# Optimization experiments

Measured on AMD Instinct MI355X. Metric: run time of the kernel, lower is better.

The kernel has to match this reference:

```python
import jax, jax.numpy as jnp
import numpy as np

N_HEADS = 16

def rotate_half(x):
    x1, x2 = jnp.split(x, 2, axis=-1)
    return jnp.concatenate([-x2, x1], axis=-1)

def setup_inputs() -> dict:
    key = jax.random.key(0)
    ks = jax.random.split(key, 6)
    dim = 2048
    B, T = 4, 2048
    x = jax.random.normal(ks[0], (B, T, dim), dtype=jnp.float32)
    pos = jnp.arange(T, dtype=jnp.float32).reshape(T, 1, 1)
    def w(k):
        return jax.random.normal(k, (dim, dim), dtype=jnp.float32) * 0.02
    return {
        "x": x, "pos": pos,
        "wq_w": w(ks[1]), "wq_b": jnp.zeros((dim,), jnp.float32),
        "wk_w": w(ks[2]), "wk_b": jnp.zeros((dim,), jnp.float32),
        "wv_w": w(ks[3]), "wv_b": jnp.zeros((dim,), jnp.float32),
        "wo_w": w(ks[4]), "wo_b": jnp.zeros((dim,), jnp.float32),
    }

def reference(x, pos, wq_w, wq_b, wk_w, wk_b, wv_w, wv_b, wo_w, wo_b):
    B, T, dim = x.shape
    H = N_HEADS
    hd = dim // H
    q = (x @ wq_w.T + wq_b).reshape(B, T, H, hd)
    k = (x @ wk_w.T + wk_b).reshape(B, T, H, hd)
    v = (x @ wv_w.T + wv_b).reshape(B, T, H, hd)
    # RoPE: freq over half the head dim, sin/cos tiled to full head dim
    freq = 1.0 / (10000.0 ** (jnp.arange(0, hd, 2, dtype=jnp.float32) / hd))  # [hd/2]
    ang = pos * freq                      # [T,1,hd/2]
    sin = jnp.concatenate([jnp.sin(ang), jnp.sin(ang)], axis=-1)  # [T,1,hd]
    cos = jnp.concatenate([jnp.cos(ang), jnp.cos(ang)], axis=-1)  # [T,1,hd]
    q = q * cos + rotate_half(q) * sin
    k = k * cos + rotate_half(k) * sin
    # [B,H,T,hd]
    q = q.transpose(0, 2, 1, 3)
    k = k.transpose(0, 2, 1, 3)
    v = v.transpose(0, 2, 1, 3)
    scale = 1.0 / np.sqrt(hd).astype(np.float32)
    attn = jnp.einsum('bhqd,bhkd->bhqk', q, k) * scale  # [B,H,T,T]
    attn = jax.nn.softmax(attn, axis=-1)
    out = jnp.einsum('bhqk,bhkd->bhqd', attn, v)        # [B,H,T,hd]
    out = out.transpose(0, 2, 1, 3).reshape(B, T, dim)
    return out @ wo_w.T + wo_b
```

## Files before the change

### kernel.cpp

```cpp
#include <hip/hip_runtime.h>


using floatx4  = __attribute__((ext_vector_type(4))) float;
using short8   = __attribute__((ext_vector_type(8))) short;
using ushortx4 = __attribute__((ext_vector_type(4))) unsigned short;

#define DEVFN static __device__ __forceinline__

DEVFN unsigned short f2bf(float f) {
  unsigned u = __builtin_bit_cast(unsigned, f);
  u += 0x7fffu + ((u >> 16) & 1u);
  return (unsigned short)(u >> 16);
}
DEVFN float bf2f(unsigned short h) {
  return __builtin_bit_cast(float, ((unsigned)h) << 16);
}

DEVFN void async_cp16(const unsigned short* g, unsigned short* l) {
  __builtin_amdgcn_global_load_lds(
      (const __attribute__((address_space(1))) void*)g,
      (__attribute__((address_space(3))) void*)l,
      16, 0, 0);
}

__global__ __launch_bounds__(256) void cast_kernel(const float4* __restrict__ in,
                                                   ushortx4* __restrict__ out) {
  long u = (long)blockIdx.x * 256 + threadIdx.x;
  float4 v = in[u];
  out[u] = (ushortx4){f2bf(v.x), f2bf(v.y), f2bf(v.z), f2bf(v.w)};
}

__global__ __launch_bounds__(256) void cs_table_kernel(const float* __restrict__ pos,
                                                       float2* __restrict__ cst) {
  int idx = blockIdx.x * 256 + threadIdx.x;
  int t = idx >> 6, j = idx & 63;
  float ang = pos[t] * exp2f(-0.20762051f * (float)j);
  cst[idx] = make_float2(cosf(ang), sinf(ang));
}

__global__ __launch_bounds__(512, 2) void qkv_gemm(
    const unsigned short* __restrict__ A,
    const unsigned short* __restrict__ Wq, const unsigned short* __restrict__ Wk,
    const unsigned short* __restrict__ Wv,
    const float* __restrict__ bq, const float* __restrict__ bk,
    const float* __restrict__ bv,
    unsigned short* __restrict__ Oq, unsigned short* __restrict__ Ok,
    unsigned short* __restrict__ Ov,
    const float2* __restrict__ cst) {
  constexpr int K = 2048;
  constexpr int NT = 64;
  __shared__ __align__(16) unsigned short lds[49152];
  const int tid = threadIdx.x;
  const int wave = tid >> 6, lane = tid & 63;
  const int ln15 = lane & 15, quad = lane >> 4;
  const int wm = wave >> 2, wn = wave & 3;
  const int bid = blockIdx.x;
  const int g = bid >> 8;
  const int b2 = bid & 255;
  const unsigned short* Bw = (g == 0) ? Wq : (g == 1) ? Wk : Wv;
  const float* bias = (g == 0) ? bq : (g == 1) ? bk : bv;
  unsigned short* Cout = (g == 0) ? Oq : (g == 1) ? Ok : Ov;
  const int xcd = b2 & 7, sl = b2 >> 3;
  const int m0 = (xcd * 4 + (sl & 3)) * 256;
  const int n0 = (sl >> 2) * 256;

  const unsigned short *srcA0, *srcA1, *srcB0, *srcB1;
  {
    int u = tid;
    int L = u >> 3, cc = (u & 7) ^ (L & 7);
    int row = L * 2 + (cc >> 2), col = (cc & 3) * 8;
    srcA0 = A + (long)(m0 + row) * K + col;
    srcB0 = Bw + (long)(n0 + row) * K + col;
  }
  {
    int u = tid + 512;
    int L = u >> 3, cc = (u & 7) ^ (L & 7);
    int row = L * 2 + (cc >> 2), col = (cc & 3) * 8;
    srcA1 = A + (long)(m0 + row) * K + col;
    srcB1 = Bw + (long)(n0 + row) * K + col;
  }
  const int sdst = wave * 512;

#define STAGE_G(t, bufp)                                                \
  do {                                                                  \
    async_cp16(srcA0 + (long)(t) * 32, (bufp) + sdst);                  \
    async_cp16(srcA1 + (long)(t) * 32, (bufp) + 4096 + sdst);           \
    async_cp16(srcB0 + (long)(t) * 32, (bufp) + 8192 + sdst);           \
    async_cp16(srcB1 + (long)(t) * 32, (bufp) + 12288 + sdst);          \
  } while (0)

  int offA[8], offB[4];
#pragma unroll
  for (int mi = 0; mi < 8; ++mi) {
    int row = wm * 128 + mi * 16 + ln15;
    int line = row >> 1, cc = (row & 1) * 4 + quad;
    offA[mi] = line * 64 + (cc ^ (line & 7)) * 8;
  }
#pragma unroll
  for (int nj = 0; nj < 4; ++nj) {
    int row = wn * 64 + nj * 16 + ln15;
    int line = row >> 1, cc = (row & 1) * 4 + quad;
    offB[nj] = 8192 + line * 64 + (cc ^ (line & 7)) * 8;
  }

  floatx4 acc[8][4];
#pragma unroll
  for (int i = 0; i < 8; ++i)
#pragma unroll
    for (int j = 0; j < 4; ++j) acc[i][j] = (floatx4){0.f, 0.f, 0.f, 0.f};

  unsigned short* const bA0 = lds;
  unsigned short* const bA1 = lds + 16384;
  unsigned short* const bA2 = lds + 32768;

  STAGE_G(0, bA0);
  STAGE_G(1, bA1);
  asm volatile("s_waitcnt vmcnt(4)" ::: "memory");
  __builtin_amdgcn_s_barrier();

  int cb = 0;
  for (int t = 0; t < NT; ++t) {
    unsigned short* cur = (cb == 0) ? bA0 : ((cb == 1) ? bA1 : bA2);
    if (t < NT - 2) {
      int nb = cb ? cb - 1 : 2;
      unsigned short* nxt = (nb == 0) ? bA0 : ((nb == 1) ? bA1 : bA2);
      STAGE_G(t + 2, nxt);
    }
    short8 af[8], bf4[4];
#pragma unroll
    for (int mi = 0; mi < 8; ++mi) af[mi] = *(const short8*)(cur + offA[mi]);
#pragma unroll
    for (int nj = 0; nj < 4; ++nj) bf4[nj] = *(const short8*)(cur + offB[nj]);
    __builtin_amdgcn_s_setprio(1);
#pragma unroll
    for (int mi = 0; mi < 8; ++mi)
#pragma unroll
      for (int nj = 0; nj < 4; ++nj)
        acc[mi][nj] = __builtin_amdgcn_mfma_f32_16x16x32_bf16(af[mi], bf4[nj],
                                                              acc[mi][nj], 0, 0, 0);
    __builtin_amdgcn_s_setprio(0);
    if (t < NT - 2) {
      asm volatile("s_waitcnt vmcnt(4)" ::: "memory");
    } else if (t == NT - 2) {
      asm volatile("s_waitcnt vmcnt(0)" ::: "memory");
    }
    __builtin_amdgcn_s_barrier();
    cb = (cb == 2) ? 0 : cb + 1;
  }
#undef STAGE_G

  const int b_ = m0 >> 11;
  const int t0m = m0 & 2047;
  const int h0 = n0 >> 7;

  if (g == 2) {
#pragma unroll
    for (int rnd = 0; rnd < 2; ++rnd) {
      __syncthreads();
      if (wm == rnd) {
#pragma unroll
        for (int nj = 0; nj < 4; ++nj) {
          int nloc = wn * 64 + nj * 16 + ln15;
          float bv = bias[n0 + nloc];
#pragma unroll
          for (int mi = 0; mi < 8; ++mi)
#pragma unroll
            for (int r = 0; r < 4; ++r) {
              int tl = mi * 16 + quad * 4 + r;
              int phys = (tl >> 3) ^ (nloc & 15);
              lds[nloc * 128 + phys * 8 + (tl & 7)] = f2bf(acc[mi][nj][r] + bv);
            }
        }
      }
      __syncthreads();
#pragma unroll
      for (int j = 0; j < 8; ++j) {
        int u = j * 512 + tid;
        int nloc = u >> 4, c = u & 15;
        int phys = c ^ (nloc & 15);
        int h = h0 + (nloc >> 7), d = nloc & 127;
        *(short8*)(Cout +
                   ((((long)(b_ * 16 + h)) << 7) + d) * 2048 + t0m + rnd * 128 + c * 8) =
            *(const short8*)(lds + nloc * 128 + phys * 8);
      }
    }
  } else {
#pragma unroll
    for (int rnd = 0; rnd < 2; ++rnd) {
      __syncthreads();
      if (wm == rnd) {
#pragma unroll
        for (int nj = 0; nj < 4; ++nj) {
          int nloc = wn * 64 + nj * 16 + ln15;
          float bv = bias[n0 + nloc];
#pragma unroll
          for (int mi = 0; mi < 8; ++mi)
#pragma unroll
            for (int r = 0; r < 4; ++r) {
              int tl = mi * 16 + quad * 4 + r;
              int phys = (nloc >> 3) ^ (tl & 15);
              lds[tl * 256 + phys * 8 + (nloc & 7)] = f2bf(acc[mi][nj][r] + bv);
            }
        }
      }
      __syncthreads();
#pragma unroll
      for (int j = 0; j < 8; ++j) {
        int u = j * 512 + tid;
        int tl = u >> 5, c = u & 31;
        int phys = c ^ (tl & 15);
        int hh = h0 + (c >> 4);
        int tt = t0m + rnd * 128 + tl;
        int cl = c & 15;
        int cp = (cl < 8) ? c + 8 : c - 8;
        int physp = cp ^ (tl & 15);
        short8 s8 = *(const short8*)(lds + tl * 256 + phys * 8);
        short8 p8 = *(const short8*)(lds + tl * 256 + physp * 8);
        const float2* ct = cst + tt * 64 + (cl & 7) * 8;
        short8 o8;
#pragma unroll
        for (int e = 0; e < 8; ++e) {
          float2 cs = ct[e];
          float x = bf2f((unsigned short)s8[e]);
          float y = bf2f((unsigned short)p8[e]);
          float v = (cl < 8) ? (x * cs.x - y * cs.y) : (x * cs.x + y * cs.y);
          o8[e] = (short)f2bf(v);
        }
        *(short8*)(Cout + ((((long)(b_ * 16 + hh)) << 11) + tt) * 128 + cl * 8) = o8;
      }
    }
  }
}

__global__ __launch_bounds__(512, 2) void gemm_wo(const unsigned short* __restrict__ A,
                                                  const unsigned short* __restrict__ Bw,
                                                  const float* __restrict__ bias,
                                                  float* __restrict__ Cout) {
  constexpr int K = 2048;
  constexpr int NT = 64;
  __shared__ __align__(16) unsigned short lds[49152];
  const int tid = threadIdx.x;
  const int wave = tid >> 6, lane = tid & 63;
  const int ln15 = lane & 15, quad = lane >> 4;
  const int wm = wave >> 2, wn = wave & 3;
  const int bid = blockIdx.x;
  const int xcd = bid & 7, sl = bid >> 3;
  const int m0 = (xcd * 4 + (sl & 3)) * 256;
  const int n0 = (sl >> 2) * 256;

  const unsigned short *srcA0, *srcA1, *srcB0, *srcB1;
  {
    int u = tid;
    int L = u >> 3, cc = (u & 7) ^ (L & 7);
    int row = L * 2 + (cc >> 2), col = (cc & 3) * 8;
    srcA0 = A + (long)(m0 + row) * K + col;
    srcB0 = Bw + (long)(n0 + row) * K + col;
  }
  {
    int u = tid + 512;
    int L = u >> 3, cc = (u & 7) ^ (L & 7);
    int row = L * 2 + (cc >> 2), col = (cc & 3) * 8;
    srcA1 = A + (long)(m0 + row) * K + col;
    srcB1 = Bw + (long)(n0 + row) * K + col;
  }
  const int sdst = wave * 512;

#define STAGE_G(t, bufp)                                                \
  do {                                                                  \
    async_cp16(srcA0 + (long)(t) * 32, (bufp) + sdst);                  \
    async_cp16(srcA1 + (long)(t) * 32, (bufp) + 4096 + sdst);           \
    async_cp16(srcB0 + (long)(t) * 32, (bufp) + 8192 + sdst);           \
    async_cp16(srcB1 + (long)(t) * 32, (bufp) + 12288 + sdst);          \
  } while (0)

  int offA[8], offB[4];
#pragma unroll
  for (int mi = 0; mi < 8; ++mi) {
    int row = wm * 128 + mi * 16 + ln15;
    int line = row >> 1, cc = (row & 1) * 4 + quad;
    offA[mi] = line * 64 + (cc ^ (line & 7)) * 8;
  }
#pragma unroll
  for (int nj = 0; nj < 4; ++nj) {
    int row = wn * 64 + nj * 16 + ln15;
    int line = row >> 1, cc = (row & 1) * 4 + quad;
    offB[nj] = 8192 + line * 64 + (cc ^ (line & 7)) * 8;
  }

  floatx4 acc[8][4];
#pragma unroll
  for (int i = 0; i < 8; ++i)
#pragma unroll
    for (int j = 0; j < 4; ++j) acc[i][j] = (floatx4){0.f, 0.f, 0.f, 0.f};

  unsigned short* const bA0 = lds;
  unsigned short* const bA1 = lds + 16384;
  unsigned short* const bA2 = lds + 32768;

  STAGE_G(0, bA0);
  STAGE_G(1, bA1);
  asm volatile("s_waitcnt vmcnt(4)" ::: "memory");
  __builtin_amdgcn_s_barrier();

  int cb = 0;
  for (int t = 0; t < NT; ++t) {
    unsigned short* cur = (cb == 0) ? bA0 : ((cb == 1) ? bA1 : bA2);
    if (t < NT - 2) {
      int nb = cb ? cb - 1 : 2;
      unsigned short* nxt = (nb == 0) ? bA0 : ((nb == 1) ? bA1 : bA2);
      STAGE_G(t + 2, nxt);
    }
    short8 af[8], bf4[4];
#pragma unroll
    for (int mi = 0; mi < 8; ++mi) af[mi] = *(const short8*)(cur + offA[mi]);
#pragma unroll
    for (int nj = 0; nj < 4; ++nj) bf4[nj] = *(const short8*)(cur + offB[nj]);
    __builtin_amdgcn_s_setprio(1);
#pragma unroll
    for (int mi = 0; mi < 8; ++mi)
#pragma unroll
      for (int nj = 0; nj < 4; ++nj)
        acc[mi][nj] = __builtin_amdgcn_mfma_f32_16x16x32_bf16(af[mi], bf4[nj],
                                                              acc[mi][nj], 0, 0, 0);
    __builtin_amdgcn_s_setprio(0);
    if (t < NT - 2) {
      asm volatile("s_waitcnt vmcnt(4)" ::: "memory");
    } else if (t == NT - 2) {
      asm volatile("s_waitcnt vmcnt(0)" ::: "memory");
    }
    __builtin_amdgcn_s_barrier();
    cb = (cb == 2) ? 0 : cb + 1;
  }
#undef STAGE_G

  float* lf = (float*)lds;
#pragma unroll
  for (int rnd = 0; rnd < 4; ++rnd) {
    __syncthreads();
    if (wm == (rnd >> 1)) {
#pragma unroll
      for (int nj = 0; nj < 4; ++nj) {
        int nloc = wn * 64 + nj * 16 + ln15;
        float bv = bias[n0 + nloc];
#pragma unroll
        for (int mh = 0; mh < 4; ++mh) {
          int mi = (rnd & 1) * 4 + mh;
#pragma unroll
          for (int r = 0; r < 4; ++r) {
            int tl = mh * 16 + quad * 4 + r;
            int phys = (nloc >> 2) ^ (tl & 15);
            lf[tl * 256 + phys * 4 + (nloc & 3)] = acc[mi][nj][r] + bv;
          }
        }
      }
    }
    __syncthreads();
#pragma unroll
    for (int j = 0; j < 8; ++j) {
      int u = j * 512 + tid;
      int tl = u >> 6, c = u & 63;
      int phys = c ^ (tl & 15);
      int m = m0 + rnd * 64 + tl;
      *(floatx4*)(Cout + (long)m * 2048 + n0 + c * 4) =
          *(const floatx4*)(lf + tl * 256 + phys * 4);
    }
  }
}

__global__ __launch_bounds__(512, 2) void flash_kernel(
    const unsigned short* __restrict__ Q,
    const unsigned short* __restrict__ Kmat,
    const unsigned short* __restrict__ Vt,
    unsigned short* __restrict__ Out) {
  constexpr int T = 2048;
  constexpr float SCALE = 0.08838834764831845f;
  __shared__ __align__(16) unsigned short lds[49152];

  const int tid = threadIdx.x;
  const int wave = tid >> 6, lane = tid & 63;
  const int ln15 = lane & 15, quad = lane >> 4;
  const int l7 = ln15 & 7;
  const int bid = blockIdx.x;
  const int xcd = bid & 7, sl = bid >> 3;
  const int bh = xcd * 8 + (sl >> 3);
  const int q0 = (sl & 7) * 256;

  const unsigned short* Qb = Q + (long)bh * T * 128;
  const unsigned short* Kb = Kmat + (long)bh * T * 128;
  const unsigned short* Vb = Vt + (long)bh * 128 * T;
  unsigned short* pw = lds + 32768 + wave * 2048;

  short8 qf[2][4];
#pragma unroll
  for (int mi = 0; mi < 2; ++mi)
#pragma unroll
    for (int ks = 0; ks < 4; ++ks)
      qf[mi][ks] = *(const short8*)(Qb + (long)(q0 + wave * 32 + mi * 16 + ln15) * 128 +
                                    ks * 32 + quad * 8);

#define STAGE_KV(t, kdst, vdst)                                                  \
  do {                                                                           \
    _Pragma("unroll") for (int j = 0; j < 2; ++j) {                              \
      int u = j * 512 + tid;                                                     \
      int row = u >> 4;                                                          \
      int c = (u & 15) ^ (row & 15);                                             \
      async_cp16(Kb + (long)((t) * 64 + row) * 128 + c * 8,                      \
                 (kdst) + (j * 512 + wave * 64) * 8);                            \
    }                                                                            \
    _Pragma("unroll") for (int j = 0; j < 2; ++j) {                              \
      int u = j * 512 + tid;                                                     \
      int row = u >> 3;                                                          \
      int c = (u & 7) ^ (row & 7);                                               \
      async_cp16(Vb + (long)row * T + (t) * 64 + c * 8,                          \
                 (vdst) + (j * 512 + wave * 64) * 8);                            \
    }                                                                            \
  } while (0)

  STAGE_KV(0, lds, lds + 16384);
  asm volatile("s_waitcnt vmcnt(0)" ::: "memory");
  __syncthreads();

  floatx4 oacc[2][8];
#pragma unroll
  for (int mi = 0; mi < 2; ++mi)
#pragma unroll
    for (int nj = 0; nj < 8; ++nj) oacc[mi][nj] = (floatx4){0.f, 0.f, 0.f, 0.f};
  float mst[2][4], lsp[2][4];
#pragma unroll
  for (int mi = 0; mi < 2; ++mi)
#pragma unroll
    for (int r = 0; r < 4; ++r) { mst[mi][r] = -1e30f; lsp[mi][r] = 0.f; }

  for (int t = 0; t < 32; ++t) {
    unsigned short* kc = lds + (t & 1) * 8192;
    unsigned short* vc = lds + 16384 + (t & 1) * 8192;
    if (t < 31) {
      unsigned short* kn = lds + ((t + 1) & 1) * 8192;
      unsigned short* vn = lds + 16384 + ((t + 1) & 1) * 8192;
      STAGE_KV(t + 1, kn, vn);
    }

    floatx4 sacc[2][4];
#pragma unroll
    for (int mi = 0; mi < 2; ++mi)
#pragma unroll
      for (int ni = 0; ni < 4; ++ni) sacc[mi][ni] = (floatx4){0.f, 0.f, 0.f, 0.f};
#pragma unroll
    for (int ks = 0; ks < 4; ++ks) {
      short8 bfr[4];
#pragma unroll
      for (int ni = 0; ni < 4; ++ni) {
        int row = ni * 16 + ln15;
        int phys = (ks * 4 + quad) ^ ln15;
        bfr[ni] = *(const short8*)(kc + row * 128 + phys * 8);
      }
      __builtin_amdgcn_s_setprio(1);
#pragma unroll
      for (int mi = 0; mi < 2; ++mi)
#pragma unroll
        for (int ni = 0; ni < 4; ++ni)
          sacc[mi][ni] = __builtin_amdgcn_mfma_f32_16x16x32_bf16(qf[mi][ks], bfr[ni],
                                                                 sacc[mi][ni], 0, 0, 0);
      __builtin_amdgcn_s_setprio(0);
    }

#pragma unroll
    for (int mi = 0; mi < 2; ++mi)
#pragma unroll
      for (int r = 0; r < 4; ++r) {
        float mx = fmaxf(fmaxf(sacc[mi][0][r], sacc[mi][1][r]),
                         fmaxf(sacc[mi][2][r], sacc[mi][3][r]));
#pragma unroll
        for (int off = 1; off < 16; off <<= 1) mx = fmaxf(mx, __shfl_xor(mx, off, 16));
        mx *= SCALE;
        float mold = mst[mi][r];
        float mnew = fmaxf(mold, mx);
        float alpha = __expf(mold - mnew);
        float rs = 0.f;
#pragma unroll
        for (int ni = 0; ni < 4; ++ni) {
          float p = __expf(sacc[mi][ni][r] * SCALE - mnew);
          sacc[mi][ni][r] = p;
          rs += p;
        }
        mst[mi][r] = mnew;
        lsp[mi][r] = lsp[mi][r] * alpha + rs;
#pragma unroll
        for (int nj = 0; nj < 8; ++nj) oacc[mi][nj][r] *= alpha;
      }

#pragma unroll
    for (int mi = 0; mi < 2; ++mi)
#pragma unroll
      for (int ni = 0; ni < 4; ++ni) {
        int cc = ni * 2 + (ln15 >> 3);
#pragma unroll
        for (int r = 0; r < 4; ++r) {
          int m = mi * 16 + quad * 4 + r;
          pw[m * 64 + (cc ^ (m & 7)) * 8 + l7] = f2bf(sacc[mi][ni][r]);
        }
      }

#pragma unroll
    for (int ks = 0; ks < 2; ++ks) {
      short8 af[2], bv[8];
#pragma unroll
      for (int mi = 0; mi < 2; ++mi) {
        int phys = (ks * 4 + quad) ^ l7;
        af[mi] = *(const short8*)(pw + (mi * 16 + ln15) * 64 + phys * 8);
      }
#pragma unroll
      for (int nj = 0; nj < 8; ++nj) {
        int row = nj * 16 + ln15;
        int phys = (ks * 4 + quad) ^ (row & 7);
        bv[nj] = *(const short8*)(vc + row * 64 + phys * 8);
      }
      __builtin_amdgcn_s_setprio(1);
#pragma unroll
      for (int mi = 0; mi < 2; ++mi)
#pragma unroll
        for (int nj = 0; nj < 8; ++nj)
          oacc[mi][nj] = __builtin_amdgcn_mfma_f32_16x16x32_bf16(af[mi], bv[nj],
                                                                 oacc[mi][nj], 0, 0, 0);
      __builtin_amdgcn_s_setprio(0);
    }

    asm volatile("s_waitcnt vmcnt(0)" ::: "memory");
    __syncthreads();
  }
#undef STAGE_KV

  float rinv[2][4];
#pragma unroll
  for (int mi = 0; mi < 2; ++mi)
#pragma unroll
    for (int r = 0; r < 4; ++r) {
      float l = lsp[mi][r];
#pragma unroll
      for (int off = 1; off < 16; off <<= 1) l += __shfl_xor(l, off, 16);
      rinv[mi][r] = 1.f / l;
    }
#pragma unroll
  for (int mi = 0; mi < 2; ++mi)
#pragma unroll
    for (int nj = 0; nj < 8; ++nj)
#pragma unroll
      for (int r = 0; r < 4; ++r)
        lds[(wave * 32 + mi * 16 + quad * 4 + r) * 128 + nj * 16 + ln15] =
            f2bf(oacc[mi][nj][r] * rinv[mi][r]);
  __syncthreads();
  const int b = bh >> 4, h = bh & 15;
  long obase = ((long)(b * T + q0) << 11) + h * 128;
#pragma unroll
  for (int j = 0; j < 8; ++j) {
    int u = j * 512 + tid;
    int r = u >> 4, c = u & 15;
    *(short8*)(Out + obase + ((long)r << 11) + c * 8) =
        *(const short8*)(lds + r * 128 + c * 8);
  }
}

extern "C" void kernel_launch(void* const* d_in, const int* in_sizes, int n_in,
                              void* d_out, int out_size, void* d_ws, size_t ws_size,
                              hipStream_t stream) {
  const float* x    = (const float*)d_in[0];
  const float* pos  = (const float*)d_in[1];
  const float* wq_w = (const float*)d_in[2];
  const float* wq_b = (const float*)d_in[3];
  const float* wk_w = (const float*)d_in[4];
  const float* wk_b = (const float*)d_in[5];
  const float* wv_w = (const float*)d_in[6];
  const float* wv_b = (const float*)d_in[7];
  const float* wo_w = (const float*)d_in[8];
  const float* wo_b = (const float*)d_in[9];

  unsigned short* xb  = (unsigned short*)d_ws;
  unsigned short* wqb = xb  + (1u << 24);
  unsigned short* wkb = wqb + (1u << 22);
  unsigned short* wvb = wkb + (1u << 22);
  unsigned short* wob = wvb + (1u << 22);
  unsigned short* qb  = wob + (1u << 22);
  unsigned short* kb  = qb  + (1u << 24);
  unsigned short* vtb = kb  + (1u << 24);
  unsigned short* ab  = vtb + (1u << 24);
  float2* cst = (float2*)ab;

  cast_kernel<<<16384, 256, 0, stream>>>((const float4*)x, (ushortx4*)xb);
  cast_kernel<<<4096, 256, 0, stream>>>((const float4*)wq_w, (ushortx4*)wqb);
  cast_kernel<<<4096, 256, 0, stream>>>((const float4*)wk_w, (ushortx4*)wkb);
  cast_kernel<<<4096, 256, 0, stream>>>((const float4*)wv_w, (ushortx4*)wvb);
  cast_kernel<<<4096, 256, 0, stream>>>((const float4*)wo_w, (ushortx4*)wob);
  cs_table_kernel<<<512, 256, 0, stream>>>(pos, cst);

  qkv_gemm<<<768, 512, 0, stream>>>(xb, wqb, wkb, wvb, wq_b, wk_b, wv_b,
                                    qb, kb, vtb, cst);
  flash_kernel<<<512, 512, 0, stream>>>(qb, kb, vtb, ab);
  gemm_wo<<<256, 512, 0, stream>>>(ab, wob, wo_b, (float*)d_out);
}
```

Before: 675.9 us.

## Fuse cast kernels, single-buffer K in flash attention, use exp2 softmax

Merges the five cast launches and the sin/cos table launch into one prep kernel to cut launch overhead. In flash attention, K is single-buffered, with the next tile's K load issued after the QK MMAs behind a barrier. This shrinks LDS from 96KB to 80KB, and launch bounds are raised to 4 blocks per CU to aim for higher occupancy. Softmax is switched to exp2 with the scale folded into log2e. The cost is less K prefetch overlap, an extra barrier per iteration, and tighter register limits that may cause spills.

```diff
diff --git a/kernel.cpp b/kernel.cpp
--- a/kernel.cpp
+++ b/kernel.cpp
@@ -23,19 +23,30 @@
       16, 0, 0);
 }
 
-__global__ __launch_bounds__(256) void cast_kernel(const float4* __restrict__ in,
-                                                   ushortx4* __restrict__ out) {
-  long u = (long)blockIdx.x * 256 + threadIdx.x;
-  float4 v = in[u];
-  out[u] = (ushortx4){f2bf(v.x), f2bf(v.y), f2bf(v.z), f2bf(v.w)};
-}
-
-__global__ __launch_bounds__(256) void cs_table_kernel(const float* __restrict__ pos,
-                                                       float2* __restrict__ cst) {
-  int idx = blockIdx.x * 256 + threadIdx.x;
-  int t = idx >> 6, j = idx & 63;
-  float ang = pos[t] * exp2f(-0.20762051f * (float)j);
-  cst[idx] = make_float2(cosf(ang), sinf(ang));
+__global__ __launch_bounds__(256) void prep_kernel(
+    const float4* __restrict__ x, const float4* __restrict__ wq,
+    const float4* __restrict__ wk, const float4* __restrict__ wv,
+    const float4* __restrict__ wo, const float* __restrict__ pos,
+    ushortx4* __restrict__ xb, ushortx4* __restrict__ wqb,
+    ushortx4* __restrict__ wkb, ushortx4* __restrict__ wvb,
+    ushortx4* __restrict__ wob, float2* __restrict__ cst) {
+  int bid = blockIdx.x;
+  if (bid < 32768) {
+    const float4* in; ushortx4* out; int base;
+    if (bid < 16384)      { in = x;  out = xb;  base = 0; }
+    else if (bid < 20480) { in = wq; out = wqb; base = 16384; }
+    else if (bid < 24576) { in = wk; out = wkb; base = 20480; }
+    else if (bid < 28672) { in = wv; out = wvb; base = 24576; }
+    else                  { in = wo; out = wob; base = 28672; }
+    long u = (long)(bid - base) * 256 + threadIdx.x;
+    float4 v = in[u];
+    out[u] = (ushortx4){f2bf(v.x), f2bf(v.y), f2bf(v.z), f2bf(v.w)};
+  } else {
+    int idx = (bid - 32768) * 256 + threadIdx.x;
+    int t = idx >> 6, j = idx & 63;
+    float ang = pos[t] * exp2f(-0.20762051f * (float)j);
+    cst[idx] = make_float2(cosf(ang), sinf(ang));
+  }
 }
 
 __global__ __launch_bounds__(512, 2) void qkv_gemm(
@@ -367,14 +378,14 @@
   }
 }
 
-__global__ __launch_bounds__(512, 2) void flash_kernel(
+__global__ __launch_bounds__(512, 4) void flash_kernel(
     const unsigned short* __restrict__ Q,
     const unsigned short* __restrict__ Kmat,
     const unsigned short* __restrict__ Vt,
     unsigned short* __restrict__ Out) {
   constexpr int T = 2048;
-  constexpr float SCALE = 0.08838834764831845f;
-  __shared__ __align__(16) unsigned short lds[49152];
+  constexpr float SL2E = 0.12754228f;
+  __shared__ __align__(16) unsigned short lds[40960];
 
   const int tid = threadIdx.x;
   const int wave = tid >> 6, lane = tid & 63;
@@ -388,7 +399,7 @@
   const unsigned short* Qb = Q + (long)bh * T * 128;
   const unsigned short* Kb = Kmat + (long)bh * T * 128;
   const unsigned short* Vb = Vt + (long)bh * 128 * T;
-  unsigned short* pw = lds + 32768 + wave * 2048;
+  unsigned short* pw = lds + 24576 + wave * 2048;
 
   short8 qf[2][4];
 #pragma unroll
@@ -398,15 +409,18 @@
       qf[mi][ks] = *(const short8*)(Qb + (long)(q0 + wave * 32 + mi * 16 + ln15) * 128 +
                                     ks * 32 + quad * 8);
 
-#define STAGE_KV(t, kdst, vdst)                                                  \
+#define STAGE_K(t)                                                               \
   do {                                                                           \
     _Pragma("unroll") for (int j = 0; j < 2; ++j) {                              \
       int u = j * 512 + tid;                                                     \
       int row = u >> 4;                                                          \
       int c = (u & 15) ^ (row & 15);                                             \
       async_cp16(Kb + (long)((t) * 64 + row) * 128 + c * 8,                      \
-                 (kdst) + (j * 512 + wave * 64) * 8);                            \
+                 lds + (j * 512 + wave * 64) * 8);                               \
     }                                                                            \
+  } while (0)
+#define STAGE_V(t, vdst)                                                         \
+  do {                                                                           \
     _Pragma("unroll") for (int j = 0; j < 2; ++j) {                              \
       int u = j * 512 + tid;                                                     \
       int row = u >> 3;                                                          \
@@ -416,7 +430,8 @@
     }                                                                            \
   } while (0)
 
-  STAGE_KV(0, lds, lds + 16384);
+  STAGE_K(0);
+  STAGE_V(0, lds + 8192);
   asm volatile("s_waitcnt vmcnt(0)" ::: "memory");
   __syncthreads();
 
@@ -432,13 +447,8 @@
     for (int r = 0; r < 4; ++r) { mst[mi][r] = -1e30f; lsp[mi][r] = 0.f; }
 
   for (int t = 0; t < 32; ++t) {
-    unsigned short* kc = lds + (t & 1) * 8192;
-    unsigned short* vc = lds + 16384 + (t & 1) * 8192;
-    if (t < 31) {
-      unsigned short* kn = lds + ((t + 1) & 1) * 8192;
-      unsigned short* vn = lds + 16384 + ((t + 1) & 1) * 8192;
-      STAGE_KV(t + 1, kn, vn);
-    }
+    unsigned short* vc = lds + 8192 + (t & 1) * 8192;
+    if (t < 31) STAGE_V(t + 1, lds + 8192 + ((t + 1) & 1) * 8192);
 
     floatx4 sacc[2][4];
 #pragma unroll
@@ -452,7 +462,7 @@
       for (int ni = 0; ni < 4; ++ni) {
         int row = ni * 16 + ln15;
         int phys = (ks * 4 + quad) ^ ln15;
-        bfr[ni] = *(const short8*)(kc + row * 128 + phys * 8);
+        bfr[ni] = *(const short8*)(lds + row * 128 + phys * 8);
       }
       __builtin_amdgcn_s_setprio(1);
 #pragma unroll
@@ -464,6 +474,10 @@
       __builtin_amdgcn_s_setprio(0);
     }
 
+    __builtin_amdgcn_s_barrier();
+    __builtin_amdgcn_sched_barrier(0);
+    if (t < 31) STAGE_K(t + 1);
+
 #pragma unroll
     for (int mi = 0; mi < 2; ++mi)
 #pragma unroll
@@ -472,14 +486,14 @@
                          fmaxf(sacc[mi][2][r], sacc[mi][3][r]));
 #pragma unroll
         for (int off = 1; off < 16; off <<= 1) mx = fmaxf(mx, __shfl_xor(mx, off, 16));
-        mx *= SCALE;
+        float m2 = mx * SL2E;
         float mold = mst[mi][r];
-        float mnew = fmaxf(mold, mx);
-        float alpha = __expf(mold - mnew);
+        float mnew = fmaxf(mold, m2);
+        float alpha = exp2f(mold - mnew);
         float rs = 0.f;
 #pragma unroll
         for (int ni = 0; ni < 4; ++ni) {
-          float p = __expf(sacc[mi][ni][r] * SCALE - mnew);
+          float p = exp2f(sacc[mi][ni][r] * SL2E - mnew);
           sacc[mi][ni][r] = p;
           rs += p;
         }
@@ -528,7 +542,8 @@
     asm volatile("s_waitcnt vmcnt(0)" ::: "memory");
     __syncthreads();
   }
-#undef STAGE_KV
+#undef STAGE_K
+#undef STAGE_V
 
   float rinv[2][4];
 #pragma unroll
@@ -585,12 +600,11 @@
   unsigned short* ab  = vtb + (1u << 24);
   float2* cst = (float2*)ab;
 
-  cast_kernel<<<16384, 256, 0, stream>>>((const float4*)x, (ushortx4*)xb);
-  cast_kernel<<<4096, 256, 0, stream>>>((const float4*)wq_w, (ushortx4*)wqb);
-  cast_kernel<<<4096, 256, 0, stream>>>((const float4*)wk_w, (ushortx4*)wkb);
-  cast_kernel<<<4096, 256, 0, stream>>>((const float4*)wv_w, (ushortx4*)wvb);
-  cast_kernel<<<4096, 256, 0, stream>>>((const float4*)wo_w, (ushortx4*)wob);
-  cs_table_kernel<<<512, 256, 0, stream>>>(pos, cst);
+  prep_kernel<<<33280, 256, 0, stream>>>((const float4*)x, (const float4*)wq_w,
+                                         (const float4*)wk_w, (const float4*)wv_w,
+                                         (const float4*)wo_w, pos,
+                                         (ushortx4*)xb, (ushortx4*)wqb, (ushortx4*)wkb,
+                                         (ushortx4*)wvb, (ushortx4*)wob, cst);
 
   qkv_gemm<<<768, 512, 0, stream>>>(xb, wqb, wkb, wvb, wq_b, wk_b, wv_b,
                                     qb, kb, vtb, cst);
```

After: 1.269 ms. +87.7%, slower.
